# Kernel optimization log

Measured on AMD Instinct MI355X. Metric: run time of the kernel, lower is better.

## Reference

```python
import jax, jax.numpy as jnp
import numpy as np

N_NODES = 50000
N_EDGES = 500000
N_REL = 50


def _linear(x, w, b):
    return x @ w.T + b


def _sage(x, src, dst, w_l, b_l, w_r, n_nodes):
    # PyG SAGEConv (mean aggr): out = lin_l(mean_{j in N(i)} x_j) + lin_r(x_i)
    msg = x[src]                                            # [E, F]
    s = jax.ops.segment_sum(msg, dst, num_segments=n_nodes)  # [N, F]
    cnt = jax.ops.segment_sum(jnp.ones((src.shape[0],), x.dtype), dst, num_segments=n_nodes)
    mean = s / jnp.clip(cnt, 1.0)[:, None]
    return mean @ w_l.T + b_l + x @ w_r.T


def setup_inputs() -> dict:
    key = jax.random.key(0)
    ks = jax.random.split(key, 24)

    def g(k, shape, fan_in):
        return jax.random.normal(k, shape, dtype=jnp.float32) * (1.0 / np.sqrt(fan_in))

    x = jax.random.normal(ks[0], (N_NODES, 16), dtype=jnp.float32)
    edge_index = jax.random.randint(ks[1], (2, N_EDGES), 0, N_NODES, dtype=jnp.int32)
    y = jax.random.randint(ks[2], (N_EDGES,), 0, N_REL, dtype=jnp.int32)

    return {
        "x": x, "edge_index": edge_index, "y": y,
        # SAGEConv 1: 16 -> 64
        "w1_l": g(ks[3], (64, 16), 16), "b1": jnp.zeros((64,), jnp.float32), "w1_r": g(ks[4], (64, 16), 16),
        # SAGEConv 2: 64 -> 128
        "w2_l": g(ks[5], (128, 64), 64), "b2": jnp.zeros((128,), jnp.float32), "w2_r": g(ks[6], (128, 64), 64),
        # object_fc: 256->128->64->32->16
        "of_w1": g(ks[7], (128, 256), 256), "of_b1": jnp.zeros((128,), jnp.float32),
        "of_w2": g(ks[8], (64, 128), 128), "of_b2": jnp.zeros((64,), jnp.float32),
        "of_w3": g(ks[9], (32, 64), 64), "of_b3": jnp.zeros((32,), jnp.float32),
        "of_w4": g(ks[10], (16, 32), 32), "of_b4": jnp.zeros((16,), jnp.float32),
        # relation_fc: 16->8->4->N_REL
        "rf_w1": g(ks[11], (8, 16), 16), "rf_b1": jnp.zeros((8,), jnp.float32),
        "rf_w2": g(ks[12], (4, 8), 8), "rf_b2": jnp.zeros((4,), jnp.float32),
        "rf_w3": g(ks[13], (N_REL, 4), 4), "rf_b3": jnp.zeros((N_REL,), jnp.float32),
    }


def reference(x, edge_index, y,
              w1_l, b1, w1_r, w2_l, b2, w2_r,
              of_w1, of_b1, of_w2, of_b2, of_w3, of_b3, of_w4, of_b4,
              rf_w1, rf_b1, rf_w2, rf_b2, rf_w3, rf_b3):
    src, dst = edge_index[0], edge_index[1]
    n = x.shape[0]

    h = jax.nn.relu(_sage(x, src, dst, w1_l, b1, w1_r, n))      # [N, 64]
    h = jax.nn.relu(_sage(h, src, dst, w2_l, b2, w2_r, n))      # [N, 128]

    # Batched version of the per-edge loop: gather endpoints, concat, MLP.
    feat = jnp.concatenate([h[src], h[dst]], axis=-1)           # [E, 256]
    o = jax.nn.relu(_linear(feat, of_w1, of_b1))   # dropout = identity (eval)
    o = jax.nn.relu(_linear(o, of_w2, of_b2))
    o = jax.nn.relu(_linear(o, of_w3, of_b3))
    o = _linear(o, of_w4, of_b4)                                # [E, 16]

    r = jax.nn.relu(_linear(o, rf_w1, rf_b1))
    r = jax.nn.relu(_linear(r, rf_w2, rf_b2))
    r = _linear(r, rf_w3, rf_b3)                                # [E, N_REL]
    return r, y
```

## Files before the change

### kernel.cpp

```cpp
#include <hip/hip_runtime.h>
#include <hip/hip_bf16.h>

#define N_NODES 50000
#define N_EDGES 500000
#define N_REL   50
#define NTILES  ((N_EDGES + 63) / 64)
#define EBLOCKS 1024
#define NODE_TILES ((N_NODES + 63) / 64)

#define CNTI_OFF   0
#define STARTS_OFF (CNTI_OFF + N_NODES)
#define CURSOR_OFF (STARTS_OFF + N_NODES)
#define SRCB_OFF   (CURSOR_OFF + N_NODES)
#define PRB_OFF    (SRCB_OFF + N_EDGES)
#define H1_OFF     (PRB_OFF + N_NODES*32)
#define PLB_OFF    (H1_OFF + N_NODES*32)

typedef short short8  __attribute__((ext_vector_type(8)));
typedef short short4v __attribute__((ext_vector_type(4)));
typedef float f32x4   __attribute__((ext_vector_type(4)));
typedef float f4      __attribute__((ext_vector_type(4)));

#define MFMA16(a,b,c) __builtin_amdgcn_mfma_f32_16x16x32_bf16((a),(b),(c),0,0,0)

__device__ __forceinline__ short f2bf(float x) {
    unsigned u = __float_as_uint(x);
    unsigned r = (u + 0x7fffu + ((u >> 16) & 1u)) >> 16;
    return (short)r;
}
__device__ __forceinline__ float bf2f(short s) {
    return __uint_as_float(((unsigned)(unsigned short)s) << 16);
}

__device__ __forceinline__ short8 load_wfrag(const float* __restrict__ W, int row, int K, int k) {
    const f4* p = (const f4*)(W + (size_t)row * K + k);
    f4 a = p[0], b = p[1];
    short8 r;
    r[0] = f2bf(a[0]); r[1] = f2bf(a[1]); r[2] = f2bf(a[2]); r[3] = f2bf(a[3]);
    r[4] = f2bf(b[0]); r[5] = f2bf(b[1]); r[6] = f2bf(b[2]); r[7] = f2bf(b[3]);
    return r;
}


__global__ __launch_bounds__(256) void k_histy(
    const int* __restrict__ dst, int* __restrict__ cnt_i,
    const int* __restrict__ y, float* __restrict__ out)
{
    int e = blockIdx.x * blockDim.x + threadIdx.x;
    if (e < N_EDGES) {
        atomicAdd(&cnt_i[dst[e]], 1);
        out[(size_t)N_EDGES * N_REL + e] = (float)y[e];
    }
}

__global__ __launch_bounds__(1024) void k_scan(
    const int* __restrict__ cnt_i, int* __restrict__ starts, int* __restrict__ cursor)
{
    __shared__ int part[1024];
    const int i  = threadIdx.x;
    const int lo = i * 49;
    const int hi = min(N_NODES, lo + 49);
    int s = 0;
    for (int j = lo; j < hi; ++j) s += cnt_i[j];
    part[i] = s;
    __syncthreads();
    for (int d = 1; d < 1024; d <<= 1) {
        int v = (i >= d) ? part[i - d] : 0;
        __syncthreads();
        part[i] += v;
        __syncthreads();
    }
    int off = (i == 0) ? 0 : part[i - 1];
    for (int j = lo; j < hi; ++j) {
        starts[j] = off;
        cursor[j] = off;
        off += cnt_i[j];
    }
}

__global__ __launch_bounds__(256) void k_bucket(
    const int* __restrict__ src, const int* __restrict__ dst,
    int* __restrict__ cursor, int* __restrict__ srcb)
{
    int e = blockIdx.x * blockDim.x + threadIdx.x;
    if (e < N_EDGES) {
        int pos = atomicAdd(&cursor[dst[e]], 1);
        srcb[pos] = src[e];
    }
}

__global__ __launch_bounds__(256) void k_sage1g(
    const float* __restrict__ x, const int* __restrict__ srcb,
    const int* __restrict__ starts, const int* __restrict__ cnt_i,
    const float* __restrict__ w1_l, const float* __restrict__ b1,
    const float* __restrict__ w1_r, short* __restrict__ h1b)
{
    __shared__ short feat[64 * 40];

    const int t    = threadIdx.x;
    const int w    = t >> 6;
    const int lane = t & 63;
    const int lr   = lane & 15;
    const int lg   = lane >> 4;
    const int base = blockIdx.x * 64;

    short8 w1f;
    if (lg < 2) w1f = load_wfrag(w1_l, w * 16 + lr, 16, lg * 8);
    else        w1f = load_wfrag(w1_r, w * 16 + lr, 16, (lg - 2) * 8);

    {
        int e  = t >> 2, q = t & 3;
        int ng = base + e;
        short8 v = (short8)0;
        if (ng < N_NODES) {
            if (q < 2) {
                int st = starts[ng], c = cnt_i[ng];
                float acc[8] = {0, 0, 0, 0, 0, 0, 0, 0};
                for (int i = 0; i < c; ++i) {
                    const float* xp = x + (size_t)srcb[st + i] * 16 + q * 8;
                    f4 a = *(const f4*)xp;
                    f4 b = *(const f4*)(xp + 4);
#pragma unroll
                    for (int j = 0; j < 4; ++j) { acc[j] += a[j]; acc[4 + j] += b[j]; }
                }
                float inv = 1.0f / (float)(c > 0 ? c : 1);
#pragma unroll
                for (int j = 0; j < 8; ++j) v[j] = f2bf(acc[j] * inv);
            } else {
                f4 a = *(const f4*)(x + (size_t)ng * 16 + (q - 2) * 8);
                f4 b = *(const f4*)(x + (size_t)ng * 16 + (q - 2) * 8 + 4);
#pragma unroll
                for (int j = 0; j < 4; ++j) { v[j] = f2bf(a[j]); v[4 + j] = f2bf(b[j]); }
            }
        }
        *(short8*)&feat[e * 40 + q * 8] = v;
    }
    __syncthreads();

    f32x4 acc[4];
    f4 bia = *(const f4*)&b1[w * 16 + lg * 4];
#pragma unroll
    for (int nt = 0; nt < 4; ++nt) {
        acc[nt][0] = bia[0]; acc[nt][1] = bia[1]; acc[nt][2] = bia[2]; acc[nt][3] = bia[3];
    }
#pragma unroll
    for (int nt = 0; nt < 4; ++nt) {
        int e = nt * 16 + lr;
        short8 bf = *(const short8*)&feat[e * 40 + lg * 8];
        acc[nt] = MFMA16(w1f, bf, acc[nt]);
    }
#pragma unroll
    for (int nt = 0; nt < 4; ++nt) {
        int ng = base + nt * 16 + lr;
        if (ng < N_NODES) {
            short4v o;
#pragma unroll
            for (int r = 0; r < 4; ++r) { float v = acc[nt][r]; o[r] = f2bf(v > 0.0f ? v : 0.0f); }
            *(short4v*)&h1b[(size_t)ng * 64 + w * 16 + lg * 4] = o;
        }
    }
}

__global__ __launch_bounds__(256) void k_sage2g(
    const short* __restrict__ h1b, const int* __restrict__ srcb,
    const int* __restrict__ starts, const int* __restrict__ cnt_i,
    const float* __restrict__ w2_l, const float* __restrict__ b2,
    const float* __restrict__ w2_r, const float* __restrict__ ow1,
    short* __restrict__ plb, short* __restrict__ prb)
{
    __shared__ short feat[64 * 128];
    __shared__ short feat2[64 * 128];

    const int t    = threadIdx.x;
    const int w    = t >> 6;
    const int lane = t & 63;
    const int lr   = lane & 15;
    const int lg   = lane >> 4;
    const int base = blockIdx.x * 64;

    short8 wf[2][4];
#pragma unroll
    for (int mt = 0; mt < 2; ++mt)
#pragma unroll
        for (int kt = 0; kt < 4; ++kt) {
            int row = w * 32 + mt * 16 + lr;
            int k   = kt * 32 + lg * 8;
            wf[mt][kt] = (k < 64) ? load_wfrag(w2_r, row, 64, k)
                                  : load_wfrag(w2_l, row, 64, k - 64);
        }

    {
        int e  = t >> 2, q = t & 3;
        int ng = base + e;
        if (q < 2) {
            const short* hp = (ng < N_NODES) ? (h1b + (size_t)ng * 64 + q * 32) : nullptr;
#pragma unroll
            for (int j = 0; j < 4; ++j) {
                short8 v = hp ? *(const short8*)(hp + j * 8) : (short8)0;
                int scol = (q * 32 + j * 8) ^ ((e & 7) << 3);
                *(short8*)&feat[e * 128 + scol] = v;
            }
        } else {
            float acc[32];
#pragma unroll
            for (int j = 0; j < 32; ++j) acc[j] = 0.0f;
            int c = 0;
            if (ng < N_NODES) {
                int st = starts[ng];
                c = cnt_i[ng];
                for (int i = 0; i < c; ++i) {
                    const short8* hp = (const short8*)(h1b + (size_t)srcb[st + i] * 64 + (q - 2) * 32);
                    short8 a0 = hp[0], a1 = hp[1], a2 = hp[2], a3 = hp[3];
#pragma unroll
                    for (int j = 0; j < 8; ++j) {
                        acc[j]      += bf2f(a0[j]);
                        acc[8 + j]  += bf2f(a1[j]);
                        acc[16 + j] += bf2f(a2[j]);
                        acc[24 + j] += bf2f(a3[j]);
                    }
                }
            }
            float inv = 1.0f / (float)(c > 0 ? c : 1);
#pragma unroll
            for (int jj = 0; jj < 4; ++jj) {
                short8 v;
#pragma unroll
                for (int j = 0; j < 8; ++j) v[j] = f2bf(acc[jj * 8 + j] * inv);
                int scol = ((q - 2) * 32 + 64 + jj * 8) ^ ((e & 7) << 3);
                *(short8*)&feat[e * 128 + scol] = v;
            }
        }
    }
    __syncthreads();

    {
        f32x4 acc[2][4];
#pragma unroll
        for (int mt = 0; mt < 2; ++mt) {
            f4 bia = *(const f4*)&b2[w * 32 + mt * 16 + lg * 4];
#pragma unroll
            for (int nt = 0; nt < 4; ++nt) {
                acc[mt][nt][0] = bia[0]; acc[mt][nt][1] = bia[1];
                acc[mt][nt][2] = bia[2]; acc[mt][nt][3] = bia[3];
            }
        }
#pragma unroll
        for (int kt = 0; kt < 4; ++kt) {
            short8 bf[4];
#pragma unroll
            for (int nt = 0; nt < 4; ++nt) {
                int e = nt * 16 + lr;
                int scol = (kt * 32 + lg * 8) ^ ((e & 7) << 3);
                bf[nt] = *(const short8*)&feat[e * 128 + scol];
            }
#pragma unroll
            for (int mt = 0; mt < 2; ++mt)
#pragma unroll
                for (int nt = 0; nt < 4; ++nt)
                    acc[mt][nt] = MFMA16(wf[mt][kt], bf[nt], acc[mt][nt]);
        }
#pragma unroll
        for (int mt = 0; mt < 2; ++mt)
#pragma unroll
            for (int nt = 0; nt < 4; ++nt) {
                int e  = nt * 16 + lr;
                int n0 = w * 32 + mt * 16 + lg * 4;
                short4v s;
#pragma unroll
                for (int r = 0; r < 4; ++r) {
                    float v = acc[mt][nt][r];
                    s[r] = f2bf(v > 0.0f ? v : 0.0f);
                }
                *(short4v*)&feat2[e * 128 + (n0 ^ ((e & 7) << 3))] = s;
            }
    }
    __syncthreads();

    short8 wfL[2][4], wfR[2][4];
#pragma unroll
    for (int mt = 0; mt < 2; ++mt)
#pragma unroll
        for (int kt = 0; kt < 4; ++kt) {
            int row = w * 32 + mt * 16 + lr;
            int k   = kt * 32 + lg * 8;
            wfL[mt][kt] = load_wfrag(ow1, row, 256, k);
            wfR[mt][kt] = load_wfrag(ow1, row, 256, 128 + k);
        }
    f32x4 aL[2][4], aR[2][4];
#pragma unroll
    for (int mt = 0; mt < 2; ++mt)
#pragma unroll
        for (int nt = 0; nt < 4; ++nt) { aL[mt][nt] = (f32x4)0.0f; aR[mt][nt] = (f32x4)0.0f; }
#pragma unroll
    for (int kt = 0; kt < 4; ++kt) {
        short8 bf[4];
#pragma unroll
        for (int nt = 0; nt < 4; ++nt) {
            int e = nt * 16 + lr;
            int scol = (kt * 32 + lg * 8) ^ ((e & 7) << 3);
            bf[nt] = *(const short8*)&feat2[e * 128 + scol];
        }
#pragma unroll
        for (int mt = 0; mt < 2; ++mt)
#pragma unroll
            for (int nt = 0; nt < 4; ++nt) {
                aL[mt][nt] = MFMA16(wfL[mt][kt], bf[nt], aL[mt][nt]);
                aR[mt][nt] = MFMA16(wfR[mt][kt], bf[nt], aR[mt][nt]);
            }
    }
#pragma unroll
    for (int mt = 0; mt < 2; ++mt)
#pragma unroll
        for (int nt = 0; nt < 4; ++nt) {
            int ng = base + nt * 16 + lr;
            if (ng < N_NODES) {
                int n0 = w * 32 + mt * 16 + lg * 4;
                short4v oL, oR;
#pragma unroll
                for (int r = 0; r < 4; ++r) { oL[r] = f2bf(aL[mt][nt][r]); oR[r] = f2bf(aR[mt][nt][r]); }
                *(short4v*)&plb[(size_t)ng * 128 + n0] = oL;
                *(short4v*)&prb[(size_t)ng * 128 + n0] = oR;
            }
        }
}

__global__ __launch_bounds__(256, 4) void k_edge3(
    const short* __restrict__ plb, const short* __restrict__ prb,
    const int* __restrict__ src, const int* __restrict__ dst,
    const float* __restrict__ ob1,
    const float* __restrict__ ow2, const float* __restrict__ ob2,
    const float* __restrict__ ow3, const float* __restrict__ ob3,
    const float* __restrict__ ow4, const float* __restrict__ ob4,
    const float* __restrict__ rw1, const float* __restrict__ rb1,
    const float* __restrict__ rw2, const float* __restrict__ rb2,
    const float* __restrict__ rw3, const float* __restrict__ rb3,
    float* __restrict__ out)
{
    __shared__ short a1s[64 * 128];
    __shared__ short actB[64 * 96];
    __shared__ float sw[662];

    short* act2  = actB;
    short* act3  = actB + 64 * 64;
    float* tailf = (float*)a1s;

    const int t    = threadIdx.x;
    const int w    = t >> 6;
    const int lane = t & 63;
    const int lr   = lane & 15;
    const int lg   = lane >> 4;

    if (t < 128) sw[t]       = ob1[t];
    if (t < 64)  sw[128 + t] = ob2[t];
    if (t < 32)  sw[192 + t] = ob3[t];
    if (t < 16)  sw[224 + t] = ob4[t];
    if (t < 8)   sw[240 + t] = rb1[t];
    if (t < 4)   sw[248 + t] = rb2[t];
    if (t < 50)  sw[252 + t] = rb3[t];
    if (t < 128) sw[302 + t] = rw1[t];
    if (t < 32)  sw[430 + t] = rw2[t];
    if (t < 200) sw[462 + t] = rw3[t];

    short8 w2f[4];
#pragma unroll
    for (int kt = 0; kt < 4; ++kt)
        w2f[kt] = load_wfrag(ow2, w * 16 + lr, 128, kt * 32 + lg * 8);

    short8 w3f[2][2];
#pragma unroll
    for (int mt = 0; mt < 2; ++mt)
#pragma unroll
        for (int kt = 0; kt < 2; ++kt)
            w3f[mt][kt] = load_wfrag(ow3, mt * 16 + lr, 64, kt * 32 + lg * 8);

    short8 w4f = load_wfrag(ow4, lr, 32, lg * 8);

    __syncthreads();

    const int e = t >> 2, p = t & 3;
    short8 vl0, vl1, vl2, vl3, vr0, vr1, vr2, vr3;

#define LOADTILE(TI)                                                        \
    {                                                                       \
        int eg  = (TI) * 64 + e;                                            \
        int egc = eg < N_EDGES ? eg : N_EDGES - 1;                          \
        int sn = src[egc], dn = dst[egc];                                   \
        const short8* plp = (const short8*)(plb + (size_t)sn * 128 + p * 32); \
        const short8* prp = (const short8*)(prb + (size_t)dn * 128 + p * 32); \
        vl0 = plp[0]; vl1 = plp[1]; vl2 = plp[2]; vl3 = plp[3];             \
        vr0 = prp[0]; vr1 = prp[1]; vr2 = prp[2]; vr3 = prp[3];             \
    }

    LOADTILE(blockIdx.x)

    for (int tile = blockIdx.x; tile < NTILES; tile += EBLOCKS) {
        const int base = tile * 64;

        {
            short8 VL[4] = {vl0, vl1, vl2, vl3};
            short8 VR[4] = {vr0, vr1, vr2, vr3};
#pragma unroll
            for (int j = 0; j < 4; ++j) {
                short8 s;
#pragma unroll
                for (int i = 0; i < 8; ++i) {
                    float v = bf2f(VL[j][i]) + bf2f(VR[j][i]) + sw[p * 32 + j * 8 + i];
                    s[i] = f2bf(v > 0.0f ? v : 0.0f);
                }
                int scol = (p * 32 + j * 8) ^ ((e & 7) << 3);
                *(short8*)&a1s[e * 128 + scol] = s;
            }
        }
        __syncthreads();

        if (tile + EBLOCKS < NTILES) LOADTILE(tile + EBLOCKS)

        {
            f32x4 acc[4];
            f32x4 bia;
#pragma unroll
            for (int r = 0; r < 4; ++r) bia[r] = sw[128 + w * 16 + lg * 4 + r];
#pragma unroll
            for (int nt = 0; nt < 4; ++nt) acc[nt] = bia;
#pragma unroll
            for (int kt = 0; kt < 4; ++kt) {
#pragma unroll
                for (int nt = 0; nt < 4; ++nt) {
                    int en = nt * 16 + lr;
                    int scol = (kt * 32 + lg * 8) ^ ((en & 7) << 3);
                    short8 bf = *(const short8*)&a1s[en * 128 + scol];
                    acc[nt] = MFMA16(w2f[kt], bf, acc[nt]);
                }
            }
#pragma unroll
            for (int nt = 0; nt < 4; ++nt) {
                int en = nt * 16 + lr;
                int n0 = w * 16 + lg * 4;
                short4v s;
#pragma unroll
                for (int r = 0; r < 4; ++r) {
                    float v = acc[nt][r];
                    s[r] = f2bf(v > 0.0f ? v : 0.0f);
                }
                *(short4v*)&act2[en * 64 + (n0 ^ ((en & 7) << 3))] = s;
            }
        }
        __syncthreads();

        {
            const int e3 = w * 16 + lr;
            float* T = tailf + w * 512;

            f32x4 acc[2];
#pragma unroll
            for (int mt = 0; mt < 2; ++mt)
#pragma unroll
                for (int r = 0; r < 4; ++r) acc[mt][r] = sw[192 + mt * 16 + lg * 4 + r];
#pragma unroll
            for (int kt = 0; kt < 2; ++kt) {
                int scol = (kt * 32 + lg * 8) ^ ((e3 & 7) << 3);
                short8 bf = *(const short8*)&act2[e3 * 64 + scol];
#pragma unroll
                for (int mt = 0; mt < 2; ++mt)
                    acc[mt] = MFMA16(w3f[mt][kt], bf, acc[mt]);
            }
#pragma unroll
            for (int mt = 0; mt < 2; ++mt) {
                short4v s;
#pragma unroll
                for (int r = 0; r < 4; ++r) {
                    float v = acc[mt][r];
                    s[r] = f2bf(v > 0.0f ? v : 0.0f);
                }
                *(short4v*)&act3[e3 * 32 + mt * 16 + lg * 4] = s;
            }
            __builtin_amdgcn_wave_barrier();

            {
                short8 bf = *(const short8*)&act3[e3 * 32 + lg * 8];
                f32x4 a4;
#pragma unroll
                for (int r = 0; r < 4; ++r) a4[r] = sw[224 + lg * 4 + r];
                a4 = MFMA16(w4f, bf, a4);
#pragma unroll
                for (int r = 0; r < 4; ++r) T[lr * 17 + lg * 4 + r] = a4[r];
            }
            __builtin_amdgcn_wave_barrier();

            {
                float af[16];
#pragma unroll
                for (int f = 0; f < 16; ++f) af[f] = T[lr * 17 + f];
#pragma unroll
                for (int oo = 0; oo < 2; ++oo) {
                    int o = lg * 2 + oo;
                    float v = sw[240 + o];
#pragma unroll
                    for (int f = 0; f < 16; ++f) v += af[f] * sw[302 + o * 16 + f];
                    T[272 + lr * 9 + o] = v > 0.0f ? v : 0.0f;
                }
            }
            __builtin_amdgcn_wave_barrier();

            {
                float v = sw[248 + lg];
#pragma unroll
                for (int f = 0; f < 8; ++f) v += T[272 + lr * 9 + f] * sw[430 + lg * 8 + f];
                T[416 + lr * 5 + lg] = v > 0.0f ? v : 0.0f;
            }
            __builtin_amdgcn_wave_barrier();

            size_t obase = (size_t)(base + w * 16) * N_REL;
#pragma unroll
            for (int k2 = 0; k2 < 13; ++k2) {
                int idx = k2 * 64 + lane;
                if (idx < 16 * N_REL) {
                    int el = idx / N_REL;
                    int o  = idx - el * N_REL;
                    if (base + w * 16 + el < N_EDGES) {
                        float v = sw[252 + o];
#pragma unroll
                        for (int f = 0; f < 4; ++f) v += T[416 + el * 5 + f] * sw[462 + o * 4 + f];
                        out[obase + idx] = v;
                    }
                }
            }
        }
        __syncthreads();
    }
#undef LOADTILE
}

extern "C" void kernel_launch(void* const* d_in, const int* in_sizes, int n_in,
                              void* d_out, int out_size, void* d_ws, size_t ws_size,
                              hipStream_t stream) {
    const float* x    = (const float*)d_in[0];
    const int*   ei   = (const int*)d_in[1];
    const int*   src  = ei;
    const int*   dst  = ei + N_EDGES;
    const int*   y    = (const int*)d_in[2];
    const float* w1_l = (const float*)d_in[3];
    const float* b1   = (const float*)d_in[4];
    const float* w1_r = (const float*)d_in[5];
    const float* w2_l = (const float*)d_in[6];
    const float* b2   = (const float*)d_in[7];
    const float* w2_r = (const float*)d_in[8];
    const float* ow1  = (const float*)d_in[9];
    const float* ob1  = (const float*)d_in[10];
    const float* ow2  = (const float*)d_in[11];
    const float* ob2  = (const float*)d_in[12];
    const float* ow3  = (const float*)d_in[13];
    const float* ob3  = (const float*)d_in[14];
    const float* ow4  = (const float*)d_in[15];
    const float* ob4  = (const float*)d_in[16];
    const float* rw1  = (const float*)d_in[17];
    const float* rb1  = (const float*)d_in[18];
    const float* rw2  = (const float*)d_in[19];
    const float* rb2  = (const float*)d_in[20];
    const float* rw3  = (const float*)d_in[21];
    const float* rb3  = (const float*)d_in[22];

    float* ws     = (float*)d_ws;
    int*   cnt_i  = (int*)(ws + CNTI_OFF);
    int*   starts = (int*)(ws + STARTS_OFF);
    int*   cursor = (int*)(ws + CURSOR_OFF);
    int*   srcb   = (int*)(ws + SRCB_OFF);
    short* prb    = (short*)(ws + PRB_OFF);
    short* h1b    = (short*)(ws + H1_OFF);
    short* plb    = (short*)(ws + PLB_OFF);
    float* out    = (float*)d_out;

    hipMemsetAsync(cnt_i, 0, N_NODES * sizeof(int), stream);

    k_histy <<<(N_EDGES + 255) / 256, 256, 0, stream>>>(dst, cnt_i, y, out);
    k_scan  <<<1, 1024, 0, stream>>>(cnt_i, starts, cursor);
    k_bucket<<<(N_EDGES + 255) / 256, 256, 0, stream>>>(src, dst, cursor, srcb);

    k_sage1g<<<NODE_TILES, 256, 0, stream>>>(x, srcb, starts, cnt_i, w1_l, b1, w1_r, h1b);
    k_sage2g<<<NODE_TILES, 256, 0, stream>>>(h1b, srcb, starts, cnt_i,
                                             w2_l, b2, w2_r, ow1, plb, prb);

    k_edge3<<<EBLOCKS, 256, 0, stream>>>(
        plb, prb, src, dst,
        ob1, ow2, ob2, ow3, ob3, ow4, ob4,
        rw1, rb1, rw2, rb2, rw3, rb3, out);
}
```

Before: 411.0 us.

## Double sage2 block to 512 threads, split neighbor gather and GEMM work across more waves

Raises k_sage2g from 256 to 512 threads per 64-node tile. The neighbor mean-aggregation is now spread over four threads per half-row, each taking every fourth neighbor, with partial sums combined by xor shuffles. The two small GEMMs are repartitioned so each wave computes fewer output rows, and the left and right ow1 projections go to separate wave groups. The aim is more latency hiding for the irregular gathers and lower per-thread register pressure, at the cost of shuffle reductions and extra idle lanes for low-degree nodes.

```diff
diff --git a/kernel.cpp b/kernel.cpp
--- a/kernel.cpp
+++ b/kernel.cpp
@@ -161,7 +161,7 @@
     }
 }
 
-__global__ __launch_bounds__(256) void k_sage2g(
+__global__ __launch_bounds__(512, 4) void k_sage2g(
     const short* __restrict__ h1b, const int* __restrict__ srcb,
     const int* __restrict__ starts, const int* __restrict__ cnt_i,
     const float* __restrict__ w2_l, const float* __restrict__ b2,
@@ -178,71 +178,77 @@
     const int lg   = lane >> 4;
     const int base = blockIdx.x * 64;
 
-    short8 wf[2][4];
-#pragma unroll
-    for (int mt = 0; mt < 2; ++mt)
-#pragma unroll
-        for (int kt = 0; kt < 4; ++kt) {
-            int row = w * 32 + mt * 16 + lr;
-            int k   = kt * 32 + lg * 8;
-            wf[mt][kt] = (k < 64) ? load_wfrag(w2_r, row, 64, k)
-                                  : load_wfrag(w2_l, row, 64, k - 64);
-        }
+    short8 wf[4];
+#pragma unroll
+    for (int kt = 0; kt < 4; ++kt) {
+        int row = w * 16 + lr;
+        int k   = kt * 32 + lg * 8;
+        wf[kt] = (k < 64) ? load_wfrag(w2_r, row, 64, k)
+                          : load_wfrag(w2_l, row, 64, k - 64);
+    }
 
     {
-        int e  = t >> 2, q = t & 3;
-        int ng = base + e;
-        if (q < 2) {
-            const short* hp = (ng < N_NODES) ? (h1b + (size_t)ng * 64 + q * 32) : nullptr;
+        int e    = t >> 3;
+        int q    = t & 7;
+        int half = q & 1;
+        int par  = q >> 1;
+        int ng   = base + e;
+        float acc[32];
+#pragma unroll
+        for (int j = 0; j < 32; ++j) acc[j] = 0.0f;
+        int c = 0;
+        if (ng < N_NODES) {
+            int st = starts[ng];
+            c = cnt_i[ng];
+            for (int i = par; i < c; i += 4) {
+                const short8* hp = (const short8*)(h1b + (size_t)srcb[st + i] * 64 + half * 32);
+                short8 a0 = hp[0], a1 = hp[1], a2 = hp[2], a3 = hp[3];
+#pragma unroll
+                for (int j = 0; j < 8; ++j) {
+                    acc[j]      += bf2f(a0[j]);
+                    acc[8 + j]  += bf2f(a1[j]);
+                    acc[16 + j] += bf2f(a2[j]);
+                    acc[24 + j] += bf2f(a3[j]);
+                }
+            }
+        }
+#pragma unroll
+        for (int j = 0; j < 32; ++j) {
+            float v = acc[j];
+            v += __shfl_xor(v, 2);
+            v += __shfl_xor(v, 4);
+            acc[j] = v;
+        }
+        if (par == 0) {
+            float inv = 1.0f / (float)(c > 0 ? c : 1);
+#pragma unroll
+            for (int jj = 0; jj < 4; ++jj) {
+                short8 v;
+#pragma unroll
+                for (int j = 0; j < 8; ++j) v[j] = f2bf(acc[jj * 8 + j] * inv);
+                int scol = (half * 32 + 64 + jj * 8) ^ ((e & 7) << 3);
+                *(short8*)&feat[e * 128 + scol] = v;
+            }
+        } else if (q == 2 || q == 3) {
+            int hs = q - 2;
+            const short* hp = (ng < N_NODES) ? (h1b + (size_t)ng * 64 + hs * 32) : nullptr;
 #pragma unroll
             for (int j = 0; j < 4; ++j) {
                 short8 v = hp ? *(const short8*)(hp + j * 8) : (short8)0;
-                int scol = (q * 32 + j * 8) ^ ((e & 7) << 3);
+                int scol = (hs * 32 + j * 8) ^ ((e & 7) << 3);
                 *(short8*)&feat[e * 128 + scol] = v;
             }
-        } else {
-            float acc[32];
-#pragma unroll
-            for (int j = 0; j < 32; ++j) acc[j] = 0.0f;
-            int c = 0;
-            if (ng < N_NODES) {
-                int st = starts[ng];
-                c = cnt_i[ng];
-                for (int i = 0; i < c; ++i) {
-                    const short8* hp = (const short8*)(h1b + (size_t)srcb[st + i] * 64 + (q - 2) * 32);
-                    short8 a0 = hp[0], a1 = hp[1], a2 = hp[2], a3 = hp[3];
-#pragma unroll
-                    for (int j = 0; j < 8; ++j) {
-                        acc[j]      += bf2f(a0[j]);
-                        acc[8 + j]  += bf2f(a1[j]);
-                        acc[16 + j] += bf2f(a2[j]);
-                        acc[24 + j] += bf2f(a3[j]);
-                    }
-                }
-            }
-            float inv = 1.0f / (float)(c > 0 ? c : 1);
-#pragma unroll
-            for (int jj = 0; jj < 4; ++jj) {
-                short8 v;
-#pragma unroll
-                for (int j = 0; j < 8; ++j) v[j] = f2bf(acc[jj * 8 + j] * inv);
-                int scol = ((q - 2) * 32 + 64 + jj * 8) ^ ((e & 7) << 3);
-                *(short8*)&feat[e * 128 + scol] = v;
-            }
         }
     }
     __syncthreads();
 
     {
-        f32x4 acc[2][4];
-#pragma unroll
-        for (int mt = 0; mt < 2; ++mt) {
-            f4 bia = *(const f4*)&b2[w * 32 + mt * 16 + lg * 4];
-#pragma unroll
-            for (int nt = 0; nt < 4; ++nt) {
-                acc[mt][nt][0] = bia[0]; acc[mt][nt][1] = bia[1];
-                acc[mt][nt][2] = bia[2]; acc[mt][nt][3] = bia[3];
-            }
+        f32x4 acc[4];
+        f4 bia = *(const f4*)&b2[w * 16 + lg * 4];
+#pragma unroll
+        for (int nt = 0; nt < 4; ++nt) {
+            acc[nt][0] = bia[0]; acc[nt][1] = bia[1];
+            acc[nt][2] = bia[2]; acc[nt][3] = bia[3];
         }
 #pragma unroll
         for (int kt = 0; kt < 4; ++kt) {
@@ -254,74 +260,71 @@
                 bf[nt] = *(const short8*)&feat[e * 128 + scol];
             }
 #pragma unroll
+            for (int nt = 0; nt < 4; ++nt)
+                acc[nt] = MFMA16(wf[kt], bf[nt], acc[nt]);
+        }
+#pragma unroll
+        for (int nt = 0; nt < 4; ++nt) {
+            int e  = nt * 16 + lr;
+            int n0 = w * 16 + lg * 4;
+            short4v s;
+#pragma unroll
+            for (int r = 0; r < 4; ++r) {
+                float v = acc[nt][r];
+                s[r] = f2bf(v > 0.0f ? v : 0.0f);
+            }
+            *(short4v*)&feat2[e * 128 + (n0 ^ ((e & 7) << 3))] = s;
+        }
+    }
+    __syncthreads();
+
+    {
+        const int isR = (w >= 4);
+        const int wb  = w & 3;
+        short8 wfp[2][4];
+#pragma unroll
+        for (int mt = 0; mt < 2; ++mt)
+#pragma unroll
+            for (int kt = 0; kt < 4; ++kt) {
+                int row = wb * 32 + mt * 16 + lr;
+                int k   = kt * 32 + lg * 8 + (isR ? 128 : 0);
+                wfp[mt][kt] = load_wfrag(ow1, row, 256, k);
+            }
+        f32x4 ap[2][4];
+#pragma unroll
+        for (int mt = 0; mt < 2; ++mt)
+#pragma unroll
+            for (int nt = 0; nt < 4; ++nt) ap[mt][nt] = (f32x4)0.0f;
+#pragma unroll
+        for (int kt = 0; kt < 4; ++kt) {
+            short8 bf[4];
+#pragma unroll
+            for (int nt = 0; nt < 4; ++nt) {
+                int e = nt * 16 + lr;
+                int scol = (kt * 32 + lg * 8) ^ ((e & 7) << 3);
+                bf[nt] = *(const short8*)&feat2[e * 128 + scol];
+            }
+#pragma unroll
             for (int mt = 0; mt < 2; ++mt)
 #pragma unroll
                 for (int nt = 0; nt < 4; ++nt)
-                    acc[mt][nt] = MFMA16(wf[mt][kt], bf[nt], acc[mt][nt]);
-        }
+                    ap[mt][nt] = MFMA16(wfp[mt][kt], bf[nt], ap[mt][nt]);
+        }
+        short* outp = isR ? prb : plb;
 #pragma unroll
         for (int mt = 0; mt < 2; ++mt)
 #pragma unroll
             for (int nt = 0; nt < 4; ++nt) {
-                int e  = nt * 16 + lr;
-                int n0 = w * 32 + mt * 16 + lg * 4;
-                short4v s;
-#pragma unroll
-                for (int r = 0; r < 4; ++r) {
-                    float v = acc[mt][nt][r];
-                    s[r] = f2bf(v > 0.0f ? v : 0.0f);
-                }
-                *(short4v*)&feat2[e * 128 + (n0 ^ ((e & 7) << 3))] = s;
-            }
-    }
-    __syncthreads();
-
-    short8 wfL[2][4], wfR[2][4];
-#pragma unroll
-    for (int mt = 0; mt < 2; ++mt)
-#pragma unroll
-        for (int kt = 0; kt < 4; ++kt) {
-            int row = w * 32 + mt * 16 + lr;
-            int k   = kt * 32 + lg * 8;
-            wfL[mt][kt] = load_wfrag(ow1, row, 256, k);
-            wfR[mt][kt] = load_wfrag(ow1, row, 256, 128 + k);
-        }
-    f32x4 aL[2][4], aR[2][4];
-#pragma unroll
-    for (int mt = 0; mt < 2; ++mt)
-#pragma unroll
-        for (int nt = 0; nt < 4; ++nt) { aL[mt][nt] = (f32x4)0.0f; aR[mt][nt] = (f32x4)0.0f; }
-#pragma unroll
-    for (int kt = 0; kt < 4; ++kt) {
-        short8 bf[4];
-#pragma unroll
-        for (int nt = 0; nt < 4; ++nt) {
-            int e = nt * 16 + lr;
-            int scol = (kt * 32 + lg * 8) ^ ((e & 7) << 3);
-            bf[nt] = *(const short8*)&feat2[e * 128 + scol];
-        }
-#pragma unroll
-        for (int mt = 0; mt < 2; ++mt)
-#pragma unroll
-            for (int nt = 0; nt < 4; ++nt) {
-                aL[mt][nt] = MFMA16(wfL[mt][kt], bf[nt], aL[mt][nt]);
-                aR[mt][nt] = MFMA16(wfR[mt][kt], bf[nt], aR[mt][nt]);
-            }
-    }
-#pragma unroll
-    for (int mt = 0; mt < 2; ++mt)
-#pragma unroll
-        for (int nt = 0; nt < 4; ++nt) {
-            int ng = base + nt * 16 + lr;
-            if (ng < N_NODES) {
-                int n0 = w * 32 + mt * 16 + lg * 4;
-                short4v oL, oR;
-#pragma unroll
-                for (int r = 0; r < 4; ++r) { oL[r] = f2bf(aL[mt][nt][r]); oR[r] = f2bf(aR[mt][nt][r]); }
-                *(short4v*)&plb[(size_t)ng * 128 + n0] = oL;
-                *(short4v*)&prb[(size_t)ng * 128 + n0] = oR;
-            }
-        }
+                int ng = base + nt * 16 + lr;
+                if (ng < N_NODES) {
+                    int n0 = wb * 32 + mt * 16 + lg * 4;
+                    short4v o;
+#pragma unroll
+                    for (int r = 0; r < 4; ++r) o[r] = f2bf(ap[mt][nt][r]);
+                    *(short4v*)&outp[(size_t)ng * 128 + n0] = o;
+                }
+            }
+    }
 }
 
 __global__ __launch_bounds__(256, 4) void k_edge3(
@@ -577,7 +580,7 @@
     k_bucket<<<(N_EDGES + 255) / 256, 256, 0, stream>>>(src, dst, cursor, srcb);
 
     k_sage1g<<<NODE_TILES, 256, 0, stream>>>(x, srcb, starts, cnt_i, w1_l, b1, w1_r, h1b);
-    k_sage2g<<<NODE_TILES, 256, 0, stream>>>(h1b, srcb, starts, cnt_i,
+    k_sage2g<<<NODE_TILES, 512, 0, stream>>>(h1b, srcb, starts, cnt_i,
                                              w2_l, b2, w2_r, ow1, plb, prb);
 
     k_edge3<<<EBLOCKS, 256, 0, stream>>>(
```

Result: no change. 404.4 us (-1.6%).
